# Kernel optimization log

Hardware: AMD Instinct MI355X
Metric: run time of the kernel (lower is better)

## Reference

```python
import jax, jax.numpy as jnp
import numpy as np

N_S, N_C, N_L = 100000, 20000, 5000
E_U, E_T = 2000000, 500000
D_S, D_C, D_L, H = 64, 32, 128, 128
N_LAYERS = 3  # num_layers=2 -> ModuleList holds 3 hetero layers


def _sage(h_src, h_dst, src_idx, dst_idx, W_self, W_neigh, b, n_dst):
    # DGL SAGEConv 'mean': fc_self(h_dst) + fc_neigh(mean of in-neighbor src feats) + bias
    summed = jax.ops.segment_sum(h_src[src_idx], dst_idx, num_segments=n_dst)  # [n_dst, d]
    deg = jax.ops.segment_sum(jnp.ones((src_idx.shape[0],), h_src.dtype), dst_idx, num_segments=n_dst)
    h_neigh = summed / jnp.maximum(deg, 1.0)[:, None]
    return h_dst @ W_self + h_neigh @ W_neigh + b


def setup_inputs() -> dict:
    key = jax.random.key(0)
    ks = jax.random.split(key, 24)
    s = 0.05
    inp = {
        'feat_student': jax.random.normal(ks[0], (N_S, D_S), jnp.float32),
        'feat_concept': jax.random.normal(ks[1], (N_C, D_C), jnp.float32),
        'feat_lecture': jax.random.normal(ks[2], (N_L, D_L), jnp.float32),
        'W_fs': jax.random.normal(ks[3], (D_S, H), jnp.float32) * s,
        'b_fs': jnp.zeros((H,), jnp.float32),
        'W_fc': jax.random.normal(ks[4], (D_C, H), jnp.float32) * s,
        'b_fc': jnp.zeros((H,), jnp.float32),
        'W_fl': jax.random.normal(ks[5], (D_L, H), jnp.float32) * s,
        'b_fl': jnp.zeros((H,), jnp.float32),
        # per-layer, per-relation SAGE params (all dims 128 so they stack)
        'W_self_u': jax.random.normal(ks[6], (N_LAYERS, H, H), jnp.float32) * s,
        'W_neigh_u': jax.random.normal(ks[7], (N_LAYERS, H, H), jnp.float32) * s,
        'b_u': jnp.zeros((N_LAYERS, H), jnp.float32),
        'W_self_t': jax.random.normal(ks[8], (N_LAYERS, H, H), jnp.float32) * s,
        'W_neigh_t': jax.random.normal(ks[9], (N_LAYERS, H, H), jnp.float32) * s,
        'b_t': jnp.zeros((N_LAYERS, H), jnp.float32),
        'und_src': jax.random.randint(ks[10], (E_U,), 0, N_S, jnp.int32),
        'und_dst': jax.random.randint(ks[11], (E_U,), 0, N_C, jnp.int32),
        'tea_src': jax.random.randint(ks[12], (E_T,), 0, N_L, jnp.int32),
        'tea_dst': jax.random.randint(ks[13], (E_T,), 0, N_C, jnp.int32),
    }
    return inp


def reference(feat_student, feat_concept, feat_lecture,
              W_fs, b_fs, W_fc, b_fc, W_fl, b_fl,
              W_self_u, W_neigh_u, b_u, W_self_t, W_neigh_t, b_t,
              und_src, und_dst, tea_src, tea_dst):
    # input projections per node type
    h_s = feat_student @ W_fs + b_fs
    h_c = feat_concept @ W_fc + b_fc
    h_l = feat_lecture @ W_fl + b_fl
    n_c = h_c.shape[0]
    for i in range(N_LAYERS):
        ou = _sage(h_s, h_c, und_src, und_dst, W_self_u[i], W_neigh_u[i], b_u[i], n_c)
        ot = _sage(h_l, h_c, tea_src, tea_dst, W_self_t[i], W_neigh_t[i], b_t[i], n_c)
        # HeteroGraphConv cross-relation aggregate: 'mean' on layer 0, default 'sum' after
        h_c = (ou + ot) * (0.5 if i == 0 else 1.0)
        if i != N_LAYERS - 1:
            h_c = jax.nn.relu(h_c)  # dropout is identity in eval mode
        # student/lecture are never destination types -> features pass through
    return h_c  # [N_C, 128] concept embeddings
```

## Files before the change

kernel.cpp:

```cpp
#include <hip/hip_runtime.h>
#include <hip/hip_bf16.h>
#include <cstdint>
#include <cstddef>

#define NS_ 100000
#define NC_ 20000
#define NL_ 5000
#define EU_ 2000000
#define ET_ 500000
#define H_  128

#define NBK_ 625
#define CHK_ 3907
#define UBLK_ 512
#define TBLK_ 128
#define CAPU_ 3600
#define CAPT_ 1024
#define SEDGE_ 3712

typedef __attribute__((ext_vector_type(8))) short bs8;
typedef __attribute__((ext_vector_type(4))) float f32x4;
typedef __attribute__((ext_vector_type(2))) float v2f;

__device__ inline short bf_rne(float f) {
    unsigned u = __float_as_uint(f);
    u = (u + 0x7fffu + ((u >> 16) & 1u)) >> 16;
    return (short)u;
}
__device__ inline unsigned pack_bf16x2(float a, float b) {
    return ((unsigned)(unsigned short)bf_rne(a)) |
           (((unsigned)(unsigned short)bf_rne(b)) << 16);
}
__device__ inline float bflo(unsigned w) { return __uint_as_float(w << 16); }
__device__ inline float bfhi(unsigned w) { return __uint_as_float(w & 0xffff0000u); }

#define B_SCU UBLK_
#define B_SCT TBLK_
#define B_CVT 512
#define B_PACK 480
#define B_BC 2
#define B_WFC 16
#define B_TOTAL (B_SCU + B_SCT + B_CVT + B_PACK + B_BC + B_WFC)

__global__ __launch_bounds__(256) void prep_fused_kernel(
    const int* __restrict__ und_dst, const int* __restrict__ und_src,
    const int* __restrict__ tea_dst, const int* __restrict__ tea_src,
    unsigned* __restrict__ gcurU, unsigned* __restrict__ gcurT,
    unsigned* __restrict__ binnedU, unsigned* __restrict__ binnedT,
    const float* __restrict__ feat_s, unsigned* __restrict__ fs8,
    const float* __restrict__ feat_l, unsigned* __restrict__ flb,
    const float* __restrict__ Wsu, const float* __restrict__ Wnu,
    const float* __restrict__ Wst, const float* __restrict__ Wnt,
    const float* __restrict__ W_fs, const float* __restrict__ W_fl,
    short* __restrict__ WpL,
    const float* __restrict__ bu, const float* __restrict__ bt,
    const float* __restrict__ b_fs, const float* __restrict__ b_fl,
    float* __restrict__ bc,
    const float* __restrict__ W_fc, short* __restrict__ WpC)
{
    __shared__ unsigned smem[5760];
    const int b = blockIdx.x;
    const int tid = threadIdx.x;

    if (b < B_SCU + B_SCT) {
        const bool isU = (b < B_SCU);
        const int blk = isU ? b : (b - B_SCU);
        const int nEdge = isU ? EU_ : ET_;
        const int* dstp = isU ? und_dst : tea_dst;
        const int* srcp = isU ? und_src : tea_src;
        unsigned* gcur = isU ? gcurU : gcurT;
        unsigned* binned = isU ? binnedU : binnedT;
        const unsigned cap = isU ? CAPU_ : CAPT_;
        unsigned* sed = smem;
        unsigned* cnt = smem + 3968;
        unsigned* pre = smem + 4736;
        unsigned* par = smem + 5504;
        for (int i = tid; i < 768; i += 256) cnt[i] = 0;
        __syncthreads();
        const int start = blk * CHK_;
        const int end = min(start + CHK_, nEdge);
        for (int i = start + tid; i < end; i += 256)
            atomicAdd(&cnt[dstp[i] >> 5], 1u);
        __syncthreads();
        unsigned c0 = cnt[3 * tid], c1 = cnt[3 * tid + 1], c2 = cnt[3 * tid + 2];
        unsigned s = c0 + c1 + c2;
        par[tid] = s;
        __syncthreads();
        unsigned sum = s;
        for (int d = 1; d < 256; d <<= 1) {
            unsigned x = (tid >= d) ? par[tid - d] : 0;
            __syncthreads();
            sum += x;
            par[tid] = sum;
            __syncthreads();
        }
        unsigned p = sum - s;
        pre[3 * tid] = p;
        pre[3 * tid + 1] = p + c0;
        pre[3 * tid + 2] = p + c0 + c1;
        __syncthreads();
        for (int k = tid; k < NBK_; k += 256) {
            unsigned L = cnt[k];
            unsigned W = L ? atomicAdd(&gcur[k], L) : 0;
            if (W + L > cap) W = cap - L;
            cnt[k] = k * cap + W - pre[k];
        }
        __syncthreads();
        for (int i = start + tid; i < end; i += 256) {
            int d = dstp[i];
            unsigned k = (unsigned)d >> 5;
            unsigned e = (unsigned)srcp[i] | ((unsigned)(d & 31) << 17) | (k << 22);
            unsigned pos = atomicAdd(&pre[k], 1u);
            sed[pos] = e;
        }
        __syncthreads();
        const int n = end - start;
        for (int i = tid; i < n; i += 256) {
            unsigned e = sed[i];
            binned[cnt[e >> 22] + i] = e & 0x3FFFFFu;
        }
    } else if (b < B_SCU + B_SCT + B_CVT) {
        int i = (b - B_SCU - B_SCT) * 256 + tid;
        const int stride = B_CVT * 256;
        const int nS = NS_ * 16;
        const int nTot = nS + NL_ * 64;
        for (; i < nTot; i += stride) {
            if (i < nS) {
                const float4 v = ((const float4*)feat_s)[i];
                unsigned r = __builtin_amdgcn_cvt_pk_fp8_f32(v.x, v.y, 0, false);
                r = __builtin_amdgcn_cvt_pk_fp8_f32(v.z, v.w, r, true);
                fs8[i] = r;
            } else {
                int j = i - nS;
                float2 v = ((const float2*)feat_l)[j];
                flb[j] = pack_bf16x2(v.x, v.y);
            }
        }
    } else if (b < B_SCU + B_SCT + B_CVT + B_PACK) {
        int i = (b - B_SCU - B_SCT - B_CVT) * 256 + tid;
        int j = i & 7;
        int lane = (i >> 3) & 63;
        int nt = (i >> 9) & 7;
        int ktAll = i >> 12;
        int l = ktAll / 10;
        int kt = ktAll - l * 10;
        int k = kt * 32 + (lane >> 4) * 8 + j;
        int n = nt * 16 + (lane & 15);
        const size_t WL = (size_t)l * H_ * H_;
        float v;
        if (k < 128) {
            v = Wsu[WL + k * H_ + n] + Wst[WL + k * H_ + n];
        } else if (k < 192) {
            int a = k - 128;
            v = 0.f;
            for (int t = 0; t < 128; t++) v += W_fs[a * H_ + t] * Wnu[WL + t * H_ + n];
        } else {
            int a = k - 192;
            v = 0.f;
            for (int t = 0; t < 128; t++) v += W_fl[a * H_ + t] * Wnt[WL + t * H_ + n];
        }
        WpL[i] = bf_rne(v);
    } else if (b < B_SCU + B_SCT + B_CVT + B_PACK + B_BC) {
        int i = (b - B_SCU - B_SCT - B_CVT - B_PACK) * 256 + tid;
        if (i < 3 * H_) {
            int l = i >> 7, c = i & 127;
            const size_t WL = (size_t)l * H_ * H_;
            float v = bu[i] + bt[i];
            for (int j2 = 0; j2 < 128; j2++)
                v += b_fs[j2] * Wnu[WL + j2 * H_ + c] + b_fl[j2] * Wnt[WL + j2 * H_ + c];
            bc[i] = v;
        }
    } else {
        int i = (b - (B_SCU + B_SCT + B_CVT + B_PACK + B_BC)) * 256 + tid;
        int j = i & 7;
        int lane = (i >> 3) & 63;
        int nt = (i >> 9) & 7;
        int k = (lane >> 4) * 8 + j;
        int n = nt * 16 + (lane & 15);
        WpC[i] = bf_rne(W_fc[k * H_ + n]);
    }
}

__global__ __launch_bounds__(256) void agg_kernel(
    const unsigned* __restrict__ gcurU, const unsigned* __restrict__ binnedU,
    const uint2* __restrict__ fs8, unsigned* __restrict__ aggFu,
    const unsigned* __restrict__ gcurT, const unsigned* __restrict__ binnedT,
    const uint4* __restrict__ flb4, unsigned* __restrict__ aggFt)
{
    __shared__ unsigned sedge[SEDGE_];
    __shared__ unsigned sh[32], soff[33], scur[32];
    const int b = blockIdx.x;
    const int tid = threadIdx.x;
    const bool isU = (b < NBK_);
    const int bb = isU ? b : (b - NBK_);
    const unsigned* binned = isU ? binnedU : binnedT;
    const unsigned cap = isU ? CAPU_ : CAPT_;
    const size_t start = (size_t)bb * cap;
    const int n = min((int)(isU ? gcurU : gcurT)[bb], (int)cap);

    if (tid < 32) sh[tid] = 0;
    __syncthreads();
    for (int i = tid; i < n; i += 256)
        atomicAdd(&sh[(binned[start + i] >> 17) & 31], 1u);
    __syncthreads();
    if (tid == 0) {
        unsigned r = 0;
        for (int j = 0; j < 32; j++) {
            unsigned v = sh[j];
            soff[j] = r;
            scur[j] = r;
            r += v;
        }
        soff[32] = r;
    }
    __syncthreads();
    for (int i = tid; i < n; i += 256) {
        unsigned p = binned[start + i];
        unsigned pos = atomicAdd(&scur[(p >> 17) & 31], 1u);
        if (pos < SEDGE_) sedge[pos] = p & 0x1FFFFu;
    }
    __syncthreads();

    const int g = tid >> 3;
    const int sub = tid & 7;
    const int gs = (int)soff[g];
    const int ge = (int)min(soff[g + 1], (unsigned)SEDGE_);
    const int c = bb * 32 + g;
    const float inv = 1.f / (float)max(ge - gs, 1);

    if (isU) {
        float a[8];
#pragma unroll
        for (int i = 0; i < 8; i++) a[i] = 0.f;
        int e = gs;
        for (; e + 2 <= ge; e += 2) {
            unsigned s0 = sedge[e], s1 = sedge[e + 1];
            uint2 w0 = fs8[(size_t)s0 * 8 + sub];
            uint2 w1 = fs8[(size_t)s1 * 8 + sub];
            v2f p0 = __builtin_amdgcn_cvt_pk_f32_fp8(w0.x, false);
            v2f p1 = __builtin_amdgcn_cvt_pk_f32_fp8(w0.x, true);
            v2f p2 = __builtin_amdgcn_cvt_pk_f32_fp8(w0.y, false);
            v2f p3 = __builtin_amdgcn_cvt_pk_f32_fp8(w0.y, true);
            a[0] += p0.x; a[1] += p0.y; a[2] += p1.x; a[3] += p1.y;
            a[4] += p2.x; a[5] += p2.y; a[6] += p3.x; a[7] += p3.y;
            p0 = __builtin_amdgcn_cvt_pk_f32_fp8(w1.x, false);
            p1 = __builtin_amdgcn_cvt_pk_f32_fp8(w1.x, true);
            p2 = __builtin_amdgcn_cvt_pk_f32_fp8(w1.y, false);
            p3 = __builtin_amdgcn_cvt_pk_f32_fp8(w1.y, true);
            a[0] += p0.x; a[1] += p0.y; a[2] += p1.x; a[3] += p1.y;
            a[4] += p2.x; a[5] += p2.y; a[6] += p3.x; a[7] += p3.y;
        }
        if (e < ge) {
            uint2 w0 = fs8[(size_t)sedge[e] * 8 + sub];
            v2f p0 = __builtin_amdgcn_cvt_pk_f32_fp8(w0.x, false);
            v2f p1 = __builtin_amdgcn_cvt_pk_f32_fp8(w0.x, true);
            v2f p2 = __builtin_amdgcn_cvt_pk_f32_fp8(w0.y, false);
            v2f p3 = __builtin_amdgcn_cvt_pk_f32_fp8(w0.y, true);
            a[0] += p0.x; a[1] += p0.y; a[2] += p1.x; a[3] += p1.y;
            a[4] += p2.x; a[5] += p2.y; a[6] += p3.x; a[7] += p3.y;
        }
        uint4 o;
        o.x = pack_bf16x2(a[0] * inv, a[1] * inv);
        o.y = pack_bf16x2(a[2] * inv, a[3] * inv);
        o.z = pack_bf16x2(a[4] * inv, a[5] * inv);
        o.w = pack_bf16x2(a[6] * inv, a[7] * inv);
        ((uint4*)aggFu)[(size_t)c * 8 + sub] = o;
    } else {
        float a[16];
#pragma unroll
        for (int i = 0; i < 16; i++) a[i] = 0.f;
        for (int e = gs; e < ge; e++) {
            unsigned src = sedge[e];
            uint4 w0 = flb4[(size_t)src * 16 + sub * 2];
            uint4 w1 = flb4[(size_t)src * 16 + sub * 2 + 1];
            a[0] += bflo(w0.x); a[1] += bfhi(w0.x);
            a[2] += bflo(w0.y); a[3] += bfhi(w0.y);
            a[4] += bflo(w0.z); a[5] += bfhi(w0.z);
            a[6] += bflo(w0.w); a[7] += bfhi(w0.w);
            a[8]  += bflo(w1.x); a[9]  += bfhi(w1.x);
            a[10] += bflo(w1.y); a[11] += bfhi(w1.y);
            a[12] += bflo(w1.z); a[13] += bfhi(w1.z);
            a[14] += bflo(w1.w); a[15] += bfhi(w1.w);
        }
        uint4 o0, o1;
        o0.x = pack_bf16x2(a[0] * inv, a[1] * inv);
        o0.y = pack_bf16x2(a[2] * inv, a[3] * inv);
        o0.z = pack_bf16x2(a[4] * inv, a[5] * inv);
        o0.w = pack_bf16x2(a[6] * inv, a[7] * inv);
        o1.x = pack_bf16x2(a[8] * inv, a[9] * inv);
        o1.y = pack_bf16x2(a[10] * inv, a[11] * inv);
        o1.z = pack_bf16x2(a[12] * inv, a[13] * inv);
        o1.w = pack_bf16x2(a[14] * inv, a[15] * inv);
        ((uint4*)aggFt)[(size_t)c * 16 + sub * 2] = o0;
        ((uint4*)aggFt)[(size_t)c * 16 + sub * 2 + 1] = o1;
    }
}

__global__ __launch_bounds__(256) void layers_fused_kernel(
    const float* __restrict__ feat_c, const short* __restrict__ WpC,
    const float* __restrict__ b_fc,
    const unsigned* __restrict__ aggFu, const unsigned* __restrict__ aggFt,
    const short* __restrict__ WpL, const float* __restrict__ bc,
    float* __restrict__ out)
{
    __shared__ short lds[4][16 * 132];
    const int tid = threadIdx.x;
    const int lane = tid & 63;
    const int wv = tid >> 6;
    const int row0 = blockIdx.x * 64 + wv * 16;
    const int q = lane >> 4;
    const int m = lane & 15;
    const int rA = min(row0 + m, NC_ - 1);
    short* tile = lds[wv];

    bs8 fuF[2], ftF[4], hcF[4];
#pragma unroll
    for (int kt = 0; kt < 2; kt++)
        fuF[kt] = *(const bs8*)(aggFu + (size_t)rA * 32 + kt * 16 + q * 4);
#pragma unroll
    for (int kt = 0; kt < 4; kt++)
        ftF[kt] = *(const bs8*)(aggFt + (size_t)rA * 64 + kt * 16 + q * 4);

    f32x4 acc[8];
#pragma unroll
    for (int i = 0; i < 8; i++) acc[i] = (f32x4){0.f, 0.f, 0.f, 0.f};
    {
        const float* xp = feat_c + (size_t)rA * 32 + q * 8;
        float4 xa = *(const float4*)xp;
        float4 xb = *(const float4*)(xp + 4);
        bs8 af;
        af[0] = bf_rne(xa.x); af[1] = bf_rne(xa.y); af[2] = bf_rne(xa.z); af[3] = bf_rne(xa.w);
        af[4] = bf_rne(xb.x); af[5] = bf_rne(xb.y); af[6] = bf_rne(xb.z); af[7] = bf_rne(xb.w);
#pragma unroll
        for (int nt = 0; nt < 8; nt++) {
            bs8 bfr = *(const bs8*)(WpC + ((size_t)nt * 64 + lane) * 8);
            acc[nt] = __builtin_amdgcn_mfma_f32_16x16x32_bf16(af, bfr, acc[nt], 0, 0, 0);
        }
    }
#pragma unroll
    for (int nt = 0; nt < 8; nt++) {
        int col = nt * 16 + m;
        float bv = b_fc[col];
#pragma unroll
        for (int r = 0; r < 4; r++)
            tile[(q * 4 + r) * 132 + col] = bf_rne(acc[nt][r] + bv);
    }
#pragma unroll
    for (int kt = 0; kt < 4; kt++)
        hcF[kt] = *(const bs8*)(tile + m * 132 + kt * 32 + q * 8);

#pragma unroll
    for (int l = 0; l < 3; l++) {
#pragma unroll
        for (int i = 0; i < 8; i++) acc[i] = (f32x4){0.f, 0.f, 0.f, 0.f};
        const short* wl = WpL + (size_t)l * 40960;
#pragma unroll
        for (int kt = 0; kt < 10; kt++) {
            bs8 af = (kt < 4) ? hcF[kt] : ((kt < 6) ? fuF[kt - 4] : ftF[kt - 6]);
            const short* wp = wl + (size_t)kt * 4096;
#pragma unroll
            for (int nt = 0; nt < 8; nt++) {
                bs8 bfr = *(const bs8*)(wp + ((size_t)nt * 64 + lane) * 8);
                acc[nt] = __builtin_amdgcn_mfma_f32_16x16x32_bf16(af, bfr, acc[nt], 0, 0, 0);
            }
        }
        const float scale = (l == 0) ? 0.5f : 1.0f;
        const float* bl = bc + l * H_;
        if (l < 2) {
#pragma unroll
            for (int nt = 0; nt < 8; nt++) {
                int col = nt * 16 + m;
                float bv = bl[col];
#pragma unroll
                for (int r = 0; r < 4; r++)
                    tile[(q * 4 + r) * 132 + col] =
                        bf_rne(fmaxf((acc[nt][r] + bv) * scale, 0.f));
            }
#pragma unroll
            for (int kt = 0; kt < 4; kt++)
                hcF[kt] = *(const bs8*)(tile + m * 132 + kt * 32 + q * 8);
        } else {
#pragma unroll
            for (int nt = 0; nt < 8; nt++) {
                int col = nt * 16 + m;
                float bv = bl[col];
#pragma unroll
                for (int r = 0; r < 4; r++) {
                    int row = row0 + q * 4 + r;
                    if (row < NC_)
                        out[(size_t)row * H_ + col] = (acc[nt][r] + bv) * scale;
                }
            }
        }
    }
}

extern "C" void kernel_launch(void* const* d_in, const int* in_sizes, int n_in,
                              void* d_out, int out_size, void* d_ws, size_t ws_size,
                              hipStream_t stream)
{
    (void)in_sizes; (void)n_in; (void)out_size; (void)ws_size;
    const float* feat_s = (const float*)d_in[0];
    const float* feat_c = (const float*)d_in[1];
    const float* feat_l = (const float*)d_in[2];
    const float* W_fs = (const float*)d_in[3];
    const float* b_fs = (const float*)d_in[4];
    const float* W_fc = (const float*)d_in[5];
    const float* b_fc = (const float*)d_in[6];
    const float* W_fl = (const float*)d_in[7];
    const float* b_fl = (const float*)d_in[8];
    const float* W_self_u  = (const float*)d_in[9];
    const float* W_neigh_u = (const float*)d_in[10];
    const float* b_u = (const float*)d_in[11];
    const float* W_self_t  = (const float*)d_in[12];
    const float* W_neigh_t = (const float*)d_in[13];
    const float* b_t = (const float*)d_in[14];
    const int* und_src = (const int*)d_in[15];
    const int* und_dst = (const int*)d_in[16];
    const int* tea_src = (const int*)d_in[17];
    const int* tea_dst = (const int*)d_in[18];
    float* out = (float*)d_out;

    char* ws = (char*)d_ws;
    size_t o = 0;
    auto alloc = [&](size_t bytes) -> char* {
        char* p = ws + o;
        o += (bytes + 255) & ~(size_t)255;
        return p;
    };
    unsigned* fs8  = (unsigned*)alloc((size_t)NS_ * 16 * 4);
    unsigned* flb  = (unsigned*)alloc((size_t)NL_ * 64 * 4);
    unsigned* aggFu = (unsigned*)alloc((size_t)NC_ * 32 * 4);
    unsigned* aggFt = (unsigned*)alloc((size_t)NC_ * 64 * 4);
    short* WpL = (short*)alloc((size_t)3 * 10 * 8 * 64 * 8 * 2);
    short* WpC = (short*)alloc((size_t)8 * 64 * 8 * 2);
    float* bc  = (float*)alloc((size_t)3 * H_ * 4);
    unsigned* gcurU = (unsigned*)alloc((size_t)NBK_ * 4);
    unsigned* gcurT = (unsigned*)alloc((size_t)NBK_ * 4);
    unsigned* binnedU = (unsigned*)alloc((size_t)NBK_ * CAPU_ * 4);
    unsigned* binnedT = (unsigned*)alloc((size_t)NBK_ * CAPT_ * 4);

    hipMemsetAsync(gcurU, 0, (size_t)((char*)binnedU - (char*)gcurU), stream);

    prep_fused_kernel<<<B_TOTAL, 256, 0, stream>>>(
        und_dst, und_src, tea_dst, tea_src, gcurU, gcurT, binnedU, binnedT,
        feat_s, fs8, feat_l, flb,
        W_self_u, W_neigh_u, W_self_t, W_neigh_t, W_fs, W_fl, WpL,
        b_u, b_t, b_fs, b_fl, bc,
        W_fc, WpC);

    agg_kernel<<<2 * NBK_, 256, 0, stream>>>(
        gcurU, binnedU, (const uint2*)fs8, aggFu,
        gcurT, binnedT, (const uint4*)flb, aggFt);

    layers_fused_kernel<<<(NC_ + 63) / 64, 256, 0, stream>>>(
        feat_c, WpC, b_fc, aggFu, aggFt, WpL, bc, out);
}
```

Before: 220.9 us.

## Split edge binning into count, column-scan, and scatter kernels

```diff
diff --git a/kernel.cpp b/kernel.cpp
--- a/kernel.cpp
+++ b/kernel.cpp
@@ -17,6 +17,7 @@
 #define CAPU_ 3600
 #define CAPT_ 1024
 #define SEDGE_ 3712
+#define SROW_ 640
 
 typedef __attribute__((ext_vector_type(8))) short bs8;
 typedef __attribute__((ext_vector_type(4))) float f32x4;
@@ -43,10 +44,8 @@
 #define B_TOTAL (B_SCU + B_SCT + B_CVT + B_PACK + B_BC + B_WFC)
 
 __global__ __launch_bounds__(256) void prep_fused_kernel(
-    const int* __restrict__ und_dst, const int* __restrict__ und_src,
-    const int* __restrict__ tea_dst, const int* __restrict__ tea_src,
-    unsigned* __restrict__ gcurU, unsigned* __restrict__ gcurT,
-    unsigned* __restrict__ binnedU, unsigned* __restrict__ binnedT,
+    const int* __restrict__ und_dst, const int* __restrict__ tea_dst,
+    unsigned* __restrict__ CUm, unsigned* __restrict__ CTm,
     const float* __restrict__ feat_s, unsigned* __restrict__ fs8,
     const float* __restrict__ feat_l, unsigned* __restrict__ flb,
     const float* __restrict__ Wsu, const float* __restrict__ Wnu,
@@ -58,7 +57,7 @@
     float* __restrict__ bc,
     const float* __restrict__ W_fc, short* __restrict__ WpC)
 {
-    __shared__ unsigned smem[5760];
+    __shared__ unsigned cnt[768];
     const int b = blockIdx.x;
     const int tid = threadIdx.x;
 
@@ -67,14 +66,7 @@
         const int blk = isU ? b : (b - B_SCU);
         const int nEdge = isU ? EU_ : ET_;
         const int* dstp = isU ? und_dst : tea_dst;
-        const int* srcp = isU ? und_src : tea_src;
-        unsigned* gcur = isU ? gcurU : gcurT;
-        unsigned* binned = isU ? binnedU : binnedT;
-        const unsigned cap = isU ? CAPU_ : CAPT_;
-        unsigned* sed = smem;
-        unsigned* cnt = smem + 3968;
-        unsigned* pre = smem + 4736;
-        unsigned* par = smem + 5504;
+        unsigned* Cm = isU ? CUm : CTm;
         for (int i = tid; i < 768; i += 256) cnt[i] = 0;
         __syncthreads();
         const int start = blk * CHK_;
@@ -82,43 +74,8 @@
         for (int i = start + tid; i < end; i += 256)
             atomicAdd(&cnt[dstp[i] >> 5], 1u);
         __syncthreads();
-        unsigned c0 = cnt[3 * tid], c1 = cnt[3 * tid + 1], c2 = cnt[3 * tid + 2];
-        unsigned s = c0 + c1 + c2;
-        par[tid] = s;
-        __syncthreads();
-        unsigned sum = s;
-        for (int d = 1; d < 256; d <<= 1) {
-            unsigned x = (tid >= d) ? par[tid - d] : 0;
-            __syncthreads();
-            sum += x;
-            par[tid] = sum;
-            __syncthreads();
-        }
-        unsigned p = sum - s;
-        pre[3 * tid] = p;
-        pre[3 * tid + 1] = p + c0;
-        pre[3 * tid + 2] = p + c0 + c1;
-        __syncthreads();
-        for (int k = tid; k < NBK_; k += 256) {
-            unsigned L = cnt[k];
-            unsigned W = L ? atomicAdd(&gcur[k], L) : 0;
-            if (W + L > cap) W = cap - L;
-            cnt[k] = k * cap + W - pre[k];
-        }
-        __syncthreads();
-        for (int i = start + tid; i < end; i += 256) {
-            int d = dstp[i];
-            unsigned k = (unsigned)d >> 5;
-            unsigned e = (unsigned)srcp[i] | ((unsigned)(d & 31) << 17) | (k << 22);
-            unsigned pos = atomicAdd(&pre[k], 1u);
-            sed[pos] = e;
-        }
-        __syncthreads();
-        const int n = end - start;
-        for (int i = tid; i < n; i += 256) {
-            unsigned e = sed[i];
-            binned[cnt[e >> 22] + i] = e & 0x3FFFFFu;
-        }
+        for (int i = tid; i < NBK_; i += 256)
+            Cm[(size_t)blk * SROW_ + i] = cnt[i];
     } else if (b < B_SCU + B_SCT + B_CVT) {
         int i = (b - B_SCU - B_SCT) * 256 + tid;
         const int stride = B_CVT * 256;
@@ -178,6 +135,145 @@
         int k = (lane >> 4) * 8 + j;
         int n = nt * 16 + (lane & 15);
         WpC[i] = bf_rne(W_fc[k * H_ + n]);
+    }
+}
+
+__global__ __launch_bounds__(256) void scan_kernel(
+    const unsigned* __restrict__ CUm, const unsigned* __restrict__ CTm,
+    unsigned* __restrict__ OUm, unsigned* __restrict__ OTm,
+    unsigned* __restrict__ gcurU, unsigned* __restrict__ gcurT)
+{
+    __shared__ unsigned part[4][64];
+    const int b = blockIdx.x;
+    const int tid = threadIdx.x;
+    const int s = tid >> 6;
+    const int kl = tid & 63;
+    const int k = b * 64 + kl;
+    const bool ok = (k < NBK_);
+
+    {
+        unsigned run = 0;
+        const int r0 = s * 128;
+        if (ok) {
+#pragma unroll 8
+            for (int r = r0; r < r0 + 128; ++r)
+                run += CUm[(size_t)r * SROW_ + k];
+        }
+        part[s][kl] = run;
+        __syncthreads();
+        unsigned base = 0;
+        for (int s2 = 0; s2 < s; ++s2) base += part[s2][kl];
+        if (ok && s == 3) gcurU[k] = base + run;
+        if (ok) {
+            unsigned acc = base;
+#pragma unroll 8
+            for (int r = r0; r < r0 + 128; ++r) {
+                unsigned c = CUm[(size_t)r * SROW_ + k];
+                OUm[(size_t)r * SROW_ + k] = acc;
+                acc += c;
+            }
+        }
+        __syncthreads();
+    }
+    {
+        unsigned run = 0;
+        const int r0 = s * 32;
+        if (ok) {
+#pragma unroll 8
+            for (int r = r0; r < r0 + 32; ++r)
+                run += CTm[(size_t)r * SROW_ + k];
+        }
+        part[s][kl] = run;
+        __syncthreads();
+        unsigned base = 0;
+        for (int s2 = 0; s2 < s; ++s2) base += part[s2][kl];
+        if (ok && s == 3) gcurT[k] = base + run;
+        if (ok) {
+            unsigned acc = base;
+#pragma unroll 8
+            for (int r = r0; r < r0 + 32; ++r) {
+                unsigned c = CTm[(size_t)r * SROW_ + k];
+                OTm[(size_t)r * SROW_ + k] = acc;
+                acc += c;
+            }
+        }
+    }
+}
+
+__global__ __launch_bounds__(256) void scatter_kernel(
+    const int* __restrict__ und_dst, const int* __restrict__ und_src,
+    const int* __restrict__ tea_dst, const int* __restrict__ tea_src,
+    const unsigned* __restrict__ CUm, const unsigned* __restrict__ CTm,
+    const unsigned* __restrict__ OUm, const unsigned* __restrict__ OTm,
+    unsigned* __restrict__ binnedU, unsigned* __restrict__ binnedT)
+{
+    __shared__ unsigned smem[5760];
+    const int b = blockIdx.x;
+    const int tid = threadIdx.x;
+    const bool isU = (b < B_SCU);
+    const int blk = isU ? b : (b - B_SCU);
+    const int nEdge = isU ? EU_ : ET_;
+    const int* dstp = isU ? und_dst : tea_dst;
+    const int* srcp = isU ? und_src : tea_src;
+    const unsigned* Cm = isU ? CUm : CTm;
+    const unsigned* Om = isU ? OUm : OTm;
+    unsigned* binned = isU ? binnedU : binnedT;
+    const unsigned cap = isU ? CAPU_ : CAPT_;
+    unsigned* sed = smem;
+    unsigned* cnt = smem + 3968;
+    unsigned* pre = smem + 4736;
+    unsigned* par = smem + 5504;
+
+    unsigned Wr[3];
+#pragma unroll
+    for (int r = 0; r < 3; r++) {
+        int k = r * 256 + tid;
+        cnt[k] = (k < NBK_) ? Cm[(size_t)blk * SROW_ + k] : 0;
+        Wr[r] = (k < NBK_) ? Om[(size_t)blk * SROW_ + k] : 0;
+    }
+    __syncthreads();
+    unsigned c0 = cnt[3 * tid], c1 = cnt[3 * tid + 1], c2 = cnt[3 * tid + 2];
+    unsigned s = c0 + c1 + c2;
+    par[tid] = s;
+    __syncthreads();
+    unsigned sum = s;
+    for (int d = 1; d < 256; d <<= 1) {
+        unsigned x = (tid >= d) ? par[tid - d] : 0;
+        __syncthreads();
+        sum += x;
+        par[tid] = sum;
+        __syncthreads();
+    }
+    unsigned p = sum - s;
+    pre[3 * tid] = p;
+    pre[3 * tid + 1] = p + c0;
+    pre[3 * tid + 2] = p + c0 + c1;
+    __syncthreads();
+#pragma unroll
+    for (int r = 0; r < 3; r++) {
+        int k = r * 256 + tid;
+        if (k < NBK_) {
+            unsigned L = cnt[k];
+            unsigned W = Wr[r];
+            if (W + L > cap) W = (L <= cap) ? cap - L : 0;
+            cnt[k] = k * cap + W - pre[k];
+        }
+    }
+    __syncthreads();
+    const int start = blk * CHK_;
+    const int end = min(start + CHK_, nEdge);
+    for (int i = start + tid; i < end; i += 256) {
+        int d = dstp[i];
+        unsigned k = (unsigned)d >> 5;
+        unsigned e = (unsigned)srcp[i] | ((unsigned)(d & 31) << 17) | (k << 22);
+        unsigned pos = atomicAdd(&pre[k], 1u);
+        sed[pos] = e;
+    }
+    __syncthreads();
+    const int n = end - start;
+    for (int i = tid; i < n; i += 256) {
+        unsigned e = sed[i];
+        binned[cnt[e >> 22] + i] = e & 0x3FFFFFu;
     }
 }
 
@@ -440,15 +536,24 @@
     unsigned* binnedU = (unsigned*)alloc((size_t)NBK_ * CAPU_ * 4);
     unsigned* binnedT = (unsigned*)alloc((size_t)NBK_ * CAPT_ * 4);
 
-    hipMemsetAsync(gcurU, 0, (size_t)((char*)binnedU - (char*)gcurU), stream);
+    unsigned* CUm = aggFt;
+    unsigned* OUm = aggFt + (size_t)UBLK_ * SROW_;
+    unsigned* CTm = aggFt + (size_t)2 * UBLK_ * SROW_;
+    unsigned* OTm = CTm + (size_t)TBLK_ * SROW_;
 
     prep_fused_kernel<<<B_TOTAL, 256, 0, stream>>>(
-        und_dst, und_src, tea_dst, tea_src, gcurU, gcurT, binnedU, binnedT,
+        und_dst, tea_dst, CUm, CTm,
         feat_s, fs8, feat_l, flb,
         W_self_u, W_neigh_u, W_self_t, W_neigh_t, W_fs, W_fl, WpL,
         b_u, b_t, b_fs, b_fl, bc,
         W_fc, WpC);
 
+    scan_kernel<<<10, 256, 0, stream>>>(CUm, CTm, OUm, OTm, gcurU, gcurT);
+
+    scatter_kernel<<<B_SCU + B_SCT, 256, 0, stream>>>(
+        und_dst, und_src, tea_dst, tea_src,
+        CUm, CTm, OUm, OTm, binnedU, binnedT);
+
     agg_kernel<<<2 * NBK_, 256, 0, stream>>>(
         gcurU, binnedU, (const uint2*)fs8, aggFu,
         gcurT, binnedT, (const uint4*)flb, aggFt);
```

Result: no change. 222.5 us (+0.7%).
